# Kernel optimization log

Hardware: AMD Instinct MI355X
Metric: run time of the kernel (lower is better)

## Reference

```python
import jax, jax.numpy as jnp
import numpy as np

N = 50000      # nodes
E = 800000     # edges (avg degree 16)
IN = 256       # in_dim == heads*hidden (so DGL residual is Identity)
H = 4          # heads
D = 64         # hidden_dim / out_dim per head
EPS = 1e-5
NEG_SLOPE_ATTN = 0.2   # DGL GATConv edge-attention leaky_relu slope
NEG_SLOPE_ACT = 0.01   # F.leaky_relu default


def gat_conv(x, src, dst, W, al, ar, b, act):
    # x: [N, H*D], W: [H*D, H*D], al/ar: [H, D], b: [H*D]
    feat = (x @ W).reshape(N, H, D)                       # [N,H,D]
    el = jnp.sum(feat * al, axis=-1)                      # [N,H]
    er = jnp.sum(feat * ar, axis=-1)                      # [N,H]
    e = jax.nn.leaky_relu(el[src] + er[dst], NEG_SLOPE_ATTN)  # [E,H]
    # segment softmax over incoming edges per destination node
    m = jax.ops.segment_max(e, dst, num_segments=N)       # [N,H]
    m = jnp.where(jnp.isfinite(m), m, 0.0)                # nodes with no in-edges
    ee = jnp.exp(e - m[dst])                              # [E,H]
    denom = jax.ops.segment_sum(ee, dst, num_segments=N)  # [N,H]
    alpha = ee / jnp.maximum(denom[dst], 1e-9)            # [E,H]
    msg = feat[src] * alpha[:, :, None]                   # [E,H,D]
    rst = jax.ops.segment_sum(msg, dst, num_segments=N)   # [N,H,D]
    rst = rst + x.reshape(N, H, D)                        # identity residual (dims match)
    rst = rst + b.reshape(1, H, D)
    if act:
        rst = jax.nn.leaky_relu(rst, NEG_SLOPE_ACT)
    return rst


def batch_norm(h, gamma, beta):
    # BatchNorm1d in training mode: batch statistics over node dim
    mu = jnp.mean(h, axis=0)
    var = jnp.var(h, axis=0)
    return (h - mu) * jax.lax.rsqrt(var + EPS) * gamma + beta


def setup_inputs():
    key = jax.random.key(0)
    ks = jax.random.split(key, 18)
    s = 1.0 / np.sqrt(IN)
    inp = {
        'x': jax.random.normal(ks[0], (N, IN), jnp.float32),
        'src': jax.random.randint(ks[1], (E,), 0, N),
        'dst': jax.random.randint(ks[2], (E,), 0, N),
    }
    names = ['W1', 'al1', 'ar1', 'b1', 'W2', 'al2', 'ar2', 'b2', 'W3', 'al3', 'ar3', 'b3']
    shapes = [(IN, H * D), (H, D), (H, D), (H * D,)] * 3
    for i, (nm, sh) in enumerate(zip(names, shapes)):
        inp[nm] = jax.random.normal(ks[3 + i], sh, jnp.float32) * s
    inp['g1'] = jnp.ones((H * D,), jnp.float32)
    inp['be1'] = jnp.zeros((H * D,), jnp.float32)
    inp['g2'] = jnp.ones((H * D,), jnp.float32)
    inp['be2'] = jnp.zeros((H * D,), jnp.float32)
    return inp


def reference(x, src, dst, W1, al1, ar1, b1, W2, al2, ar2, b2, W3, al3, ar3, b3, g1, be1, g2, be2):
    h = gat_conv(x, src, dst, W1, al1, ar1, b1, act=True).reshape(N, H * D)
    h = batch_norm(h, g1, be1)
    h = gat_conv(h, src, dst, W2, al2, ar2, b2, act=True).reshape(N, H * D)
    h = batch_norm(h, g2, be2)
    h = gat_conv(h, src, dst, W3, al3, ar3, b3, act=False)   # [N,H,D]
    return h.mean(axis=1)                                    # [N,D]
```

## Files before the change

kernel.cpp:

```cpp
#include <hip/hip_runtime.h>

constexpr int NN = 50000;
constexpr int NE = 800000;
constexpr float SLOPE_A = 0.2f;
constexpr float SLOPE_R = 0.01f;
constexpr int SCB = 196;

typedef __attribute__((ext_vector_type(8))) short bf16x8;
typedef __attribute__((ext_vector_type(4))) float f32x4;

__device__ __forceinline__ unsigned short f2bf(float f) {
    union { float f; unsigned u; } v; v.f = f;
    unsigned u = v.u;
    unsigned r = u + 0x7fffu + ((u >> 16) & 1u);
    return (unsigned short)(r >> 16);
}
__device__ __forceinline__ float bf2f(unsigned short s) {
    union { unsigned u; float f; } v; v.u = ((unsigned)s) << 16;
    return v.f;
}
__device__ __forceinline__ float bflo(unsigned u) {
    union { unsigned u; float f; } v; v.u = u << 16; return v.f;
}
__device__ __forceinline__ float bfhi(unsigned u) {
    union { unsigned u; float f; } v; v.u = u & 0xffff0000u; return v.f;
}

__global__ void k_hist(const int* __restrict__ dst, int* __restrict__ cnt) {
    int i = blockIdx.x * 256 + threadIdx.x;
    if (i < NE) atomicAdd(&cnt[dst[i]], 1);
}

__global__ void k_scan1(const int* __restrict__ cnt, int* __restrict__ loc,
                        int* __restrict__ bsum) {
    __shared__ int sh[256];
    int t = threadIdx.x;
    int i = blockIdx.x * 256 + t;
    int v = (i < NN) ? cnt[i] : 0;
    sh[t] = v;
    __syncthreads();
    for (int off = 1; off < 256; off <<= 1) {
        int tmp = (t >= off) ? sh[t - off] : 0;
        __syncthreads();
        sh[t] += tmp;
        __syncthreads();
    }
    loc[i] = sh[t] - v;
    if (t == 255) bsum[blockIdx.x] = sh[255];
}

__global__ void k_scan2(const int* __restrict__ bsum, int* __restrict__ boff,
                        int* __restrict__ rowptr) {
    __shared__ int sh[256];
    int t = threadIdx.x;
    int v = (t < SCB) ? bsum[t] : 0;
    sh[t] = v;
    __syncthreads();
    for (int off = 1; off < 256; off <<= 1) {
        int tmp = (t >= off) ? sh[t - off] : 0;
        __syncthreads();
        sh[t] += tmp;
        __syncthreads();
    }
    if (t < SCB) boff[t] = sh[t] - v;
    if (t == 255) rowptr[NN] = sh[255];
}

__global__ void k_scan3(const int* __restrict__ loc, const int* __restrict__ boff,
                        int* __restrict__ rowptr, int* __restrict__ cursor) {
    int i = blockIdx.x * 256 + threadIdx.x;
    if (i < NN) {
        int r = loc[i] + boff[blockIdx.x];
        rowptr[i] = r;
        cursor[i] = r;
    }
}

__global__ void k_scatter(const int* __restrict__ src, const int* __restrict__ dst,
                          int* __restrict__ cursor, int* __restrict__ ssrc) {
    int i = blockIdx.x * 256 + threadIdx.x;
    if (i < NE) {
        int d = dst[i];
        int pos = atomicAdd(&cursor[d], 1);
        ssrc[pos] = src[i];
    }
}

__global__ void k_fold(const float* __restrict__ W, const float* __restrict__ sc,
                       const float* __restrict__ sh, const float* __restrict__ al,
                       const float* __restrict__ ar, unsigned short* __restrict__ Wfrag,
                       float* __restrict__ cvec, unsigned short* __restrict__ wlrfrag,
                       float* __restrict__ offlr, int has_bn) {
    int b = blockIdx.x;
    if (b < 32) {
        int gid = b * 256 + threadIdx.x;
        int lane = gid & 63;
        int frag = gid >> 6;
        int j = frag & 3, kc = (frag >> 2) & 7, w = frag >> 5;
        int mm = lane & 15, q = lane >> 4;
        int n = 64 * w + 16 * j + mm;
        int k0 = kc * 32 + q * 8;
        unsigned short o[8];
#pragma unroll
        for (int t = 0; t < 8; t++) {
            float wv = W[(size_t)(k0 + t) * 256 + n];
            if (sc) wv *= sc[k0 + t];
            o[t] = f2bf(wv);
        }
        *(uint4*)(Wfrag + (size_t)gid * 8) = *(const uint4*)o;
    } else if (has_bn && b < 288) {
        __shared__ float red[256];
        int n = b - 32, k = threadIdx.x;
        red[k] = sh[k] * W[(size_t)k * 256 + n];
        __syncthreads();
        for (int off = 128; off > 0; off >>= 1) {
            if (k < off) red[k] += red[k + off];
            __syncthreads();
        }
        if (k == 0) cvec[n] = red[0];
    } else {
        int n = b - (has_bn ? 288 : 32);
        int h = n >> 1;
        const float* a = (n & 1) ? ar : al;
        int k = threadIdx.x;
        float raw = 0.f;
#pragma unroll 8
        for (int d = 0; d < 64; d++)
            raw += W[(size_t)k * 256 + 64 * h + d] * a[h * 64 + d];
        float val = (sc ? sc[k] : 1.f) * raw;
        int kc = k >> 5, rem = k & 31, q = rem >> 3, t = rem & 7;
        wlrfrag[kc * 512 + (q * 16 + n) * 8 + t] = f2bf(val);
        wlrfrag[kc * 512 + (q * 16 + n + 8) * 8 + t] = 0;
        __shared__ float red[256];
        red[k] = sh ? sh[k] * raw : 0.f;
        __syncthreads();
        for (int off = 128; off > 0; off >>= 1) {
            if (k < off) red[k] += red[k + off];
            __syncthreads();
        }
        if (k == 0) offlr[n] = red[0];
    }
}

__launch_bounds__(256)
__global__ void k_gemm(const void* __restrict__ Araw, int af32,
                       const unsigned short* __restrict__ Wfrag,
                       const float* __restrict__ cvec,
                       const unsigned short* __restrict__ wlrfrag,
                       const float* __restrict__ offlr,
                       unsigned short* __restrict__ feat16, float* __restrict__ el,
                       float* __restrict__ er) {
    constexpr int AP = 264;
    __shared__ __align__(16) unsigned short Alds[64 * AP];
    const int tid = threadIdx.x;
    const int rowbase = blockIdx.x * 64;

    if (af32) {
        const float* A = (const float*)Araw;
        int r = tid >> 6;
        int c4 = tid & 63;
        for (int it = 0; it < 16; it++) {
            int rr = it * 4 + r;
            int gr = rowbase + rr;
            float4 v = make_float4(0.f, 0.f, 0.f, 0.f);
            if (gr < NN) v = *(const float4*)(A + (size_t)gr * 256 + c4 * 4);
            ushort4 pv;
            pv.x = f2bf(v.x); pv.y = f2bf(v.y); pv.z = f2bf(v.z); pv.w = f2bf(v.w);
            *(ushort4*)(&Alds[rr * AP + c4 * 4]) = pv;
        }
    } else {
        const unsigned short* A = (const unsigned short*)Araw;
        for (int it = 0; it < 8; it++) {
            int idx = it * 256 + tid;
            int rr = idx >> 5;
            int c16 = idx & 31;
            int gr = rowbase + rr;
            uint4 v = make_uint4(0u, 0u, 0u, 0u);
            if (gr < NN) v = *(const uint4*)(A + (size_t)gr * 256 + c16 * 8);
            *(uint4*)(&Alds[rr * AP + c16 * 8]) = v;
        }
    }
    __syncthreads();

    f32x4 acc[4][4];
    for (int i = 0; i < 4; i++)
        for (int j = 0; j < 4; j++)
            acc[i][j] = (f32x4){0.f, 0.f, 0.f, 0.f};
    f32x4 accLR[4];
    for (int i = 0; i < 4; i++) accLR[i] = (f32x4){0.f, 0.f, 0.f, 0.f};

    const int lane = tid & 63, w = tid >> 6;
    const int mm = lane & 15, q = lane >> 4;

    const unsigned short* bbase = Wfrag + ((size_t)w * 8 * 4) * 512 + (size_t)lane * 8;

#pragma unroll
    for (int kc = 0; kc < 8; kc++) {
        bf16x8 a[4], b[4];
        for (int i = 0; i < 4; i++)
            a[i] = *(const bf16x8*)(&Alds[(16 * i + mm) * AP + kc * 32 + q * 8]);
        for (int j = 0; j < 4; j++)
            b[j] = *(const bf16x8*)(bbase + (size_t)(kc * 4 + j) * 512);
        for (int i = 0; i < 4; i++)
            for (int j = 0; j < 4; j++)
                acc[i][j] = __builtin_amdgcn_mfma_f32_16x16x32_bf16(a[i], b[j], acc[i][j], 0, 0, 0);
        if (w == 0) {
            bf16x8 blr = *(const bf16x8*)(wlrfrag + kc * 512 + lane * 8);
            for (int i = 0; i < 4; i++)
                accLR[i] = __builtin_amdgcn_mfma_f32_16x16x32_bf16(a[i], blr, accLR[i], 0, 0, 0);
        }
    }
    __syncthreads();

    if (cvec) {
        float cv[4];
        for (int j = 0; j < 4; j++) cv[j] = cvec[64 * w + 16 * j + mm];
        for (int i = 0; i < 4; i++)
            for (int j = 0; j < 4; j++)
                for (int r = 0; r < 4; r++)
                    acc[i][j][r] += cv[j];
    }

    if (w == 0 && mm < 8) {
        float off = offlr[mm];
        int h = mm >> 1;
        float* dstp = (mm & 1) ? er : el;
        for (int i = 0; i < 4; i++)
            for (int r = 0; r < 4; r++) {
                int gr = rowbase + 16 * i + q * 4 + r;
                if (gr < NN) dstp[gr * 4 + h] = accLR[i][r] + off;
            }
    }

    for (int i = 0; i < 4; i++)
        for (int j = 0; j < 4; j++) {
            int gc = 64 * w + 16 * j + mm;
            for (int r = 0; r < 4; r++) {
                int rr = 16 * i + q * 4 + r;
                Alds[rr * AP + gc] = f2bf(acc[i][j][r]);
            }
        }
    __syncthreads();
    for (int it = 0; it < 8; it++) {
        int idx = it * 256 + tid;
        int rr = idx >> 5;
        int c16 = idx & 31;
        int gr = rowbase + rr;
        if (gr < NN)
            *(uint4*)(feat16 + (size_t)gr * 256 + c16 * 8) = *(const uint4*)(&Alds[rr * AP + c16 * 8]);
    }
}

__launch_bounds__(256)
__global__ void k_agg(const unsigned short* __restrict__ feat16,
                      const float* __restrict__ el, const float* __restrict__ er,
                      const int* __restrict__ rowptr, const int* __restrict__ ssrc,
                      const unsigned short* __restrict__ residh, const float* __restrict__ residf,
                      const float* __restrict__ bnscale, const float* __restrict__ bnshift,
                      int use_bn, const float* __restrict__ bias, int act,
                      unsigned short* __restrict__ outh, float* __restrict__ outf,
                      int final_mean) {
    int n = __builtin_amdgcn_readfirstlane(blockIdx.x * 4 + (threadIdx.x >> 6));
    int l = threadIdx.x & 63;
    int p = l >> 5;
    int q = l & 31;
    int c8 = q * 8;
    int hh = q >> 3;
    int wh = l & 3;
    int we = l >> 2;
    int beg = rowptr[n], end = rowptr[n + 1];
    float er_w = er[n * 4 + wh];

    float d = 0.f;
    float acc[8];
#pragma unroll
    for (int k = 0; k < 8; k++) acc[k] = 0.f;

    for (int e = beg; e < end; e += 16) {
        int widx = e + we;
        bool wv = widx < end;
        int sw = ssrc[wv ? widx : beg];
        float a = el[sw * 4 + wh];
        float sc = a + er_w;
        sc = (sc > 0.f) ? sc : SLOPE_A * sc;
        float wl = wv ? __expf(sc) : 0.f;

        int ss[8];
#pragma unroll
        for (int t = 0; t < 8; t++) {
            int idx = e + 2 * t + p;
            ss[t] = ssrc[(idx < end) ? idx : beg];
        }
        uint4 ff[8];
#pragma unroll
        for (int t = 0; t < 8; t++)
            ff[t] = *(const uint4*)(feat16 + (size_t)ss[t] * 256 + c8);

#pragma unroll
        for (int t = 0; t < 8; t++) {
            float w = __shfl(wl, (2 * t + p) * 4 + hh, 64);
            d += w;
            acc[0] += bflo(ff[t].x) * w; acc[1] += bfhi(ff[t].x) * w;
            acc[2] += bflo(ff[t].y) * w; acc[3] += bfhi(ff[t].y) * w;
            acc[4] += bflo(ff[t].z) * w; acc[5] += bfhi(ff[t].z) * w;
            acc[6] += bflo(ff[t].w) * w; acc[7] += bfhi(ff[t].w) * w;
        }
    }

    d += __shfl_xor(d, 32, 64);
#pragma unroll
    for (int k = 0; k < 8; k++) acc[k] += __shfl_xor(acc[k], 32, 64);

    float invd = 1.f / fmaxf(d, 1e-9f);
#pragma unroll
    for (int k = 0; k < 8; k++) acc[k] *= invd;

    float r[8];
    if (residf) {
        float4 r0 = *(const float4*)(residf + (size_t)n * 256 + c8);
        float4 r1 = *(const float4*)(residf + (size_t)n * 256 + c8 + 4);
        r[0] = r0.x; r[1] = r0.y; r[2] = r0.z; r[3] = r0.w;
        r[4] = r1.x; r[5] = r1.y; r[6] = r1.z; r[7] = r1.w;
    } else {
        uint4 rv = *(const uint4*)(residh + (size_t)n * 256 + c8);
        r[0] = bflo(rv.x); r[1] = bfhi(rv.x);
        r[2] = bflo(rv.y); r[3] = bfhi(rv.y);
        r[4] = bflo(rv.z); r[5] = bfhi(rv.z);
        r[6] = bflo(rv.w); r[7] = bfhi(rv.w);
    }

    if (use_bn) {
        float4 s0 = *(const float4*)(bnscale + c8);
        float4 s1 = *(const float4*)(bnscale + c8 + 4);
        float4 h0 = *(const float4*)(bnshift + c8);
        float4 h1 = *(const float4*)(bnshift + c8 + 4);
        r[0] = r[0] * s0.x + h0.x; r[1] = r[1] * s0.y + h0.y;
        r[2] = r[2] * s0.z + h0.z; r[3] = r[3] * s0.w + h0.w;
        r[4] = r[4] * s1.x + h1.x; r[5] = r[5] * s1.y + h1.y;
        r[6] = r[6] * s1.z + h1.z; r[7] = r[7] * s1.w + h1.w;
    }
    {
        float4 b0 = *(const float4*)(bias + c8);
        float4 b1 = *(const float4*)(bias + c8 + 4);
        acc[0] += r[0] + b0.x; acc[1] += r[1] + b0.y;
        acc[2] += r[2] + b0.z; acc[3] += r[3] + b0.w;
        acc[4] += r[4] + b1.x; acc[5] += r[5] + b1.y;
        acc[6] += r[6] + b1.z; acc[7] += r[7] + b1.w;
    }
    if (act) {
#pragma unroll
        for (int k = 0; k < 8; k++) acc[k] = (acc[k] > 0.f) ? acc[k] : SLOPE_R * acc[k];
    }

    if (!final_mean) {
        if (p == 0) {
            uint4 o;
            o.x = (unsigned)f2bf(acc[0]) | ((unsigned)f2bf(acc[1]) << 16);
            o.y = (unsigned)f2bf(acc[2]) | ((unsigned)f2bf(acc[3]) << 16);
            o.z = (unsigned)f2bf(acc[4]) | ((unsigned)f2bf(acc[5]) << 16);
            o.w = (unsigned)f2bf(acc[6]) | ((unsigned)f2bf(acc[7]) << 16);
            *(uint4*)(outh + (size_t)n * 256 + c8) = o;
        }
    } else {
#pragma unroll
        for (int k = 0; k < 8; k++) {
            acc[k] += __shfl_xor(acc[k], 8, 64);
            acc[k] += __shfl_xor(acc[k], 16, 64);
        }
        if (p == 0 && q < 8) {
            float4 o0 = make_float4(acc[0] * 0.25f, acc[1] * 0.25f, acc[2] * 0.25f, acc[3] * 0.25f);
            float4 o1 = make_float4(acc[4] * 0.25f, acc[5] * 0.25f, acc[6] * 0.25f, acc[7] * 0.25f);
            *(float4*)(outf + (size_t)n * 64 + c8) = o0;
            *(float4*)(outf + (size_t)n * 64 + c8 + 4) = o1;
        }
    }
}

__global__ void k_bnstats(const unsigned short* __restrict__ hh, float* __restrict__ pbuf) {
    __shared__ float ps[8 * 256];
    __shared__ float ps2[8 * 256];
    int t = threadIdx.x, b = blockIdx.x;
    int r8 = t >> 5, c32 = t & 31;
    int r0 = b * 196, r1 = min(r0 + 196, NN);
    float s[8], s2[8];
#pragma unroll
    for (int e = 0; e < 8; e++) { s[e] = 0.f; s2[e] = 0.f; }
    for (int r = r0 + r8; r < r1; r += 8) {
        uint4 v = *(const uint4*)(hh + (size_t)r * 256 + c32 * 8);
        const unsigned short* pv = (const unsigned short*)&v;
#pragma unroll
        for (int e = 0; e < 8; e++) {
            float f = bf2f(pv[e]);
            s[e] += f; s2[e] += f * f;
        }
    }
#pragma unroll
    for (int e = 0; e < 8; e++) {
        ps[r8 * 256 + c32 * 8 + e] = s[e];
        ps2[r8 * 256 + c32 * 8 + e] = s2[e];
    }
    __syncthreads();
    float ts = 0.f, ts2 = 0.f;
    for (int g = 0; g < 8; g++) { ts += ps[g * 256 + t]; ts2 += ps2[g * 256 + t]; }
    pbuf[b * 512 + t] = ts;
    pbuf[b * 512 + 256 + t] = ts2;
}

__global__ void k_bnfinal(const float* __restrict__ pbuf, const float* __restrict__ g,
                          const float* __restrict__ be, float* __restrict__ scale,
                          float* __restrict__ shift) {
    int t = threadIdx.x;
    float s = 0.f, s2 = 0.f;
    for (int b = 0; b < 256; b++) {
        s += pbuf[b * 512 + t];
        s2 += pbuf[b * 512 + 256 + t];
    }
    float mu = s * (1.f / NN);
    float var = s2 * (1.f / NN) - mu * mu;
    float rs = rsqrtf(var + 1e-5f);
    float sc = rs * g[t];
    scale[t] = sc;
    shift[t] = be[t] - mu * sc;
}

extern "C" void kernel_launch(void* const* d_in, const int* in_sizes, int n_in,
                              void* d_out, int out_size, void* d_ws, size_t ws_size,
                              hipStream_t stream) {
    const float* x   = (const float*)d_in[0];
    const int* src   = (const int*)d_in[1];
    const int* dst   = (const int*)d_in[2];
    const float* W1  = (const float*)d_in[3];
    const float* al1 = (const float*)d_in[4];
    const float* ar1 = (const float*)d_in[5];
    const float* b1  = (const float*)d_in[6];
    const float* W2  = (const float*)d_in[7];
    const float* al2 = (const float*)d_in[8];
    const float* ar2 = (const float*)d_in[9];
    const float* b2  = (const float*)d_in[10];
    const float* W3  = (const float*)d_in[11];
    const float* al3 = (const float*)d_in[12];
    const float* ar3 = (const float*)d_in[13];
    const float* b3  = (const float*)d_in[14];
    const float* g1  = (const float*)d_in[15];
    const float* be1 = (const float*)d_in[16];
    const float* g2  = (const float*)d_in[17];
    const float* be2 = (const float*)d_in[18];
    float* out = (float*)d_out;

    char* ws = (char*)d_ws;
    size_t off = 0;
    auto alloc = [&](size_t bytes) {
        void* p = ws + off;
        off += (bytes + 255) & ~(size_t)255;
        return p;
    };
    int* rowptr = (int*)alloc((NN + 1) * sizeof(int));
    int* cursor = (int*)alloc(NN * sizeof(int));
    int* cnt    = (int*)alloc(SCB * 256 * sizeof(int));
    int* loc    = (int*)alloc(SCB * 256 * sizeof(int));
    int* bsum   = (int*)alloc(SCB * sizeof(int));
    int* boff   = (int*)alloc(SCB * sizeof(int));
    int* ssrc   = (int*)alloc(NE * sizeof(int));
    unsigned short* feat16 = (unsigned short*)alloc((size_t)NN * 256 * sizeof(unsigned short));
    unsigned short* hbuf   = (unsigned short*)alloc((size_t)NN * 256 * sizeof(unsigned short));
    float* el   = (float*)alloc((size_t)NN * 4 * sizeof(float));
    float* er   = (float*)alloc((size_t)NN * 4 * sizeof(float));
    unsigned short* Wfrag1  = (unsigned short*)alloc(65536 * sizeof(unsigned short));
    unsigned short* Wfrag2  = (unsigned short*)alloc(65536 * sizeof(unsigned short));
    unsigned short* wlrfrag = (unsigned short*)alloc(4096 * sizeof(unsigned short));
    float* offlr   = (float*)alloc(16 * sizeof(float));
    float* cvec    = (float*)alloc(256 * sizeof(float));
    float* pbuf    = (float*)alloc(256 * 512 * sizeof(float));
    float* bnscale = (float*)alloc(256 * sizeof(float));
    float* bnshift = (float*)alloc(256 * sizeof(float));

    hipMemsetAsync(cnt, 0, NN * sizeof(int), stream);
    k_hist<<<(NE + 255) / 256, 256, 0, stream>>>(dst, cnt);
    k_scan1<<<SCB, 256, 0, stream>>>(cnt, loc, bsum);
    k_scan2<<<1, 256, 0, stream>>>(bsum, boff, rowptr);
    k_scan3<<<SCB, 256, 0, stream>>>(loc, boff, rowptr, cursor);
    k_scatter<<<(NE + 255) / 256, 256, 0, stream>>>(src, dst, cursor, ssrc);
    k_fold<<<40, 256, 0, stream>>>(W1, nullptr, nullptr, al1, ar1,
                                   Wfrag1, nullptr, wlrfrag, offlr, 0);

    const int GB = (NN + 63) / 64;
    const int NB = NN / 4;

    k_gemm<<<GB, 256, 0, stream>>>(x, 1, Wfrag1, nullptr, wlrfrag, offlr, feat16, el, er);
    k_agg<<<NB, 256, 0, stream>>>(feat16, el, er, rowptr, ssrc, nullptr, x,
                                  nullptr, nullptr, 0, b1, 1, hbuf, nullptr, 0);
    k_bnstats<<<256, 256, 0, stream>>>(hbuf, pbuf);
    k_bnfinal<<<1, 256, 0, stream>>>(pbuf, g1, be1, bnscale, bnshift);
    k_fold<<<296, 256, 0, stream>>>(W2, bnscale, bnshift, al2, ar2,
                                    Wfrag2, cvec, wlrfrag, offlr, 1);

    k_gemm<<<GB, 256, 0, stream>>>(hbuf, 0, Wfrag2, cvec, wlrfrag, offlr, feat16, el, er);
    k_agg<<<NB, 256, 0, stream>>>(feat16, el, er, rowptr, ssrc, hbuf, nullptr,
                                  bnscale, bnshift, 1, b2, 1, hbuf, nullptr, 0);
    k_bnstats<<<256, 256, 0, stream>>>(hbuf, pbuf);
    k_bnfinal<<<1, 256, 0, stream>>>(pbuf, g2, be2, bnscale, bnshift);
    k_fold<<<296, 256, 0, stream>>>(W3, bnscale, bnshift, al3, ar3,
                                    Wfrag2, cvec, wlrfrag, offlr, 1);

    k_gemm<<<GB, 256, 0, stream>>>(hbuf, 0, Wfrag2, cvec, wlrfrag, offlr, feat16, el, er);
    k_agg<<<NB, 256, 0, stream>>>(feat16, el, er, rowptr, ssrc, hbuf, nullptr,
                                  bnscale, bnshift, 1, b3, 0, nullptr, out, 1);
}
```

Before: 571.6 us.

## Split GAT aggregation into per-head column slices with compact indices

The aggregation kernel is restructured so each block handles 16 nodes for one 32-column slice, with the 8 slices of a node group on consecutive block indices. Each lane group computes its own head's attention weights, so the cross-lane shuffle of weights goes away. The el/er logits are stored head-major, and the sorted source indices are stored as 16-bit values since N fits. The goal is more parallelism, better L2 locality on feature gathers, and less index traffic. In exchange, index and logit reads are repeated across the slices, and the final head-mean becomes float atomics into a zero-initialised output.

```diff
diff --git a/kernel.cpp b/kernel.cpp
--- a/kernel.cpp
+++ b/kernel.cpp
@@ -77,12 +77,12 @@
 }
 
 __global__ void k_scatter(const int* __restrict__ src, const int* __restrict__ dst,
-                          int* __restrict__ cursor, int* __restrict__ ssrc) {
+                          int* __restrict__ cursor, unsigned short* __restrict__ ssrc) {
     int i = blockIdx.x * 256 + threadIdx.x;
     if (i < NE) {
         int d = dst[i];
         int pos = atomicAdd(&cursor[d], 1);
-        ssrc[pos] = src[i];
+        ssrc[pos] = (unsigned short)src[i];
     }
 }
 
@@ -228,7 +228,7 @@
         for (int i = 0; i < 4; i++)
             for (int r = 0; r < 4; r++) {
                 int gr = rowbase + 16 * i + q * 4 + r;
-                if (gr < NN) dstp[gr * 4 + h] = accLR[i][r] + off;
+                if (gr < NN) dstp[h * NN + gr] = accLR[i][r] + off;
             }
     }
 
@@ -252,126 +252,125 @@
 }
 
 __launch_bounds__(256)
-__global__ void k_agg(const unsigned short* __restrict__ feat16,
-                      const float* __restrict__ el, const float* __restrict__ er,
-                      const int* __restrict__ rowptr, const int* __restrict__ ssrc,
-                      const unsigned short* __restrict__ residh, const float* __restrict__ residf,
-                      const float* __restrict__ bnscale, const float* __restrict__ bnshift,
-                      int use_bn, const float* __restrict__ bias, int act,
-                      unsigned short* __restrict__ outh, float* __restrict__ outf,
-                      int final_mean) {
-    int n = __builtin_amdgcn_readfirstlane(blockIdx.x * 4 + (threadIdx.x >> 6));
+__global__ void k_aggs(const unsigned short* __restrict__ feat16,
+                       const float* __restrict__ el, const float* __restrict__ er,
+                       const int* __restrict__ rowptr, const unsigned short* __restrict__ ssrc,
+                       const unsigned short* __restrict__ residh, const float* __restrict__ residf,
+                       const float* __restrict__ bnscale, const float* __restrict__ bnshift,
+                       int use_bn, const float* __restrict__ bias, int act,
+                       unsigned short* __restrict__ outh, float* __restrict__ outf,
+                       int final_mean) {
+    int b = blockIdx.x;
+    int slice = b & 7;
+    int ng = b >> 3;
     int l = threadIdx.x & 63;
-    int p = l >> 5;
-    int q = l & 31;
-    int c8 = q * 8;
-    int hh = q >> 3;
-    int wh = l & 3;
-    int we = l >> 2;
+    int w = threadIdx.x >> 6;
+    int j = l >> 4;
+    int r = l & 15;
+    int es = r >> 2;
+    int ck = r & 3;
+    int n = ng * 16 + w * 4 + j;
+    int h = slice >> 1;
+    int coff = slice * 32 + ck * 8;
+
     int beg = rowptr[n], end = rowptr[n + 1];
-    float er_w = er[n * 4 + wh];
+    float er_h = er[h * NN + n];
+    const float* elh = el + h * NN;
 
     float d = 0.f;
     float acc[8];
 #pragma unroll
     for (int k = 0; k < 8; k++) acc[k] = 0.f;
 
-    for (int e = beg; e < end; e += 16) {
-        int widx = e + we;
-        bool wv = widx < end;
-        int sw = ssrc[wv ? widx : beg];
-        float a = el[sw * 4 + wh];
-        float sc = a + er_w;
-        sc = (sc > 0.f) ? sc : SLOPE_A * sc;
-        float wl = wv ? __expf(sc) : 0.f;
-
-        int ss[8];
-#pragma unroll
-        for (int t = 0; t < 8; t++) {
-            int idx = e + 2 * t + p;
+    for (int e0 = beg; e0 < end; e0 += 16) {
+        int ss[4];
+#pragma unroll
+        for (int t = 0; t < 4; t++) {
+            int idx = e0 + t * 4 + es;
             ss[t] = ssrc[(idx < end) ? idx : beg];
         }
-        uint4 ff[8];
-#pragma unroll
-        for (int t = 0; t < 8; t++)
-            ff[t] = *(const uint4*)(feat16 + (size_t)ss[t] * 256 + c8);
-
-#pragma unroll
-        for (int t = 0; t < 8; t++) {
-            float w = __shfl(wl, (2 * t + p) * 4 + hh, 64);
-            d += w;
-            acc[0] += bflo(ff[t].x) * w; acc[1] += bfhi(ff[t].x) * w;
-            acc[2] += bflo(ff[t].y) * w; acc[3] += bfhi(ff[t].y) * w;
-            acc[4] += bflo(ff[t].z) * w; acc[5] += bfhi(ff[t].z) * w;
-            acc[6] += bflo(ff[t].w) * w; acc[7] += bfhi(ff[t].w) * w;
-        }
-    }
-
-    d += __shfl_xor(d, 32, 64);
-#pragma unroll
-    for (int k = 0; k < 8; k++) acc[k] += __shfl_xor(acc[k], 32, 64);
+        float aa[4];
+#pragma unroll
+        for (int t = 0; t < 4; t++) aa[t] = elh[ss[t]];
+        uint4 ff[4];
+#pragma unroll
+        for (int t = 0; t < 4; t++)
+            ff[t] = *(const uint4*)(feat16 + (size_t)ss[t] * 256 + coff);
+#pragma unroll
+        for (int t = 0; t < 4; t++) {
+            int idx = e0 + t * 4 + es;
+            float sc = aa[t] + er_h;
+            sc = (sc > 0.f) ? sc : SLOPE_A * sc;
+            float wg = (idx < end) ? __expf(sc) : 0.f;
+            d += wg;
+            acc[0] += bflo(ff[t].x) * wg; acc[1] += bfhi(ff[t].x) * wg;
+            acc[2] += bflo(ff[t].y) * wg; acc[3] += bfhi(ff[t].y) * wg;
+            acc[4] += bflo(ff[t].z) * wg; acc[5] += bfhi(ff[t].z) * wg;
+            acc[6] += bflo(ff[t].w) * wg; acc[7] += bfhi(ff[t].w) * wg;
+        }
+    }
+
+    d += __shfl_xor(d, 4, 64);
+    d += __shfl_xor(d, 8, 64);
+#pragma unroll
+    for (int k = 0; k < 8; k++) {
+        acc[k] += __shfl_xor(acc[k], 4, 64);
+        acc[k] += __shfl_xor(acc[k], 8, 64);
+    }
 
     float invd = 1.f / fmaxf(d, 1e-9f);
 #pragma unroll
     for (int k = 0; k < 8; k++) acc[k] *= invd;
 
-    float r[8];
+    float rr[8];
     if (residf) {
-        float4 r0 = *(const float4*)(residf + (size_t)n * 256 + c8);
-        float4 r1 = *(const float4*)(residf + (size_t)n * 256 + c8 + 4);
-        r[0] = r0.x; r[1] = r0.y; r[2] = r0.z; r[3] = r0.w;
-        r[4] = r1.x; r[5] = r1.y; r[6] = r1.z; r[7] = r1.w;
+        float4 r0 = *(const float4*)(residf + (size_t)n * 256 + coff);
+        float4 r1 = *(const float4*)(residf + (size_t)n * 256 + coff + 4);
+        rr[0] = r0.x; rr[1] = r0.y; rr[2] = r0.z; rr[3] = r0.w;
+        rr[4] = r1.x; rr[5] = r1.y; rr[6] = r1.z; rr[7] = r1.w;
     } else {
-        uint4 rv = *(const uint4*)(residh + (size_t)n * 256 + c8);
-        r[0] = bflo(rv.x); r[1] = bfhi(rv.x);
-        r[2] = bflo(rv.y); r[3] = bfhi(rv.y);
-        r[4] = bflo(rv.z); r[5] = bfhi(rv.z);
-        r[6] = bflo(rv.w); r[7] = bfhi(rv.w);
-    }
-
+        uint4 rv = *(const uint4*)(residh + (size_t)n * 256 + coff);
+        rr[0] = bflo(rv.x); rr[1] = bfhi(rv.x);
+        rr[2] = bflo(rv.y); rr[3] = bfhi(rv.y);
+        rr[4] = bflo(rv.z); rr[5] = bfhi(rv.z);
+        rr[6] = bflo(rv.w); rr[7] = bfhi(rv.w);
+    }
     if (use_bn) {
-        float4 s0 = *(const float4*)(bnscale + c8);
-        float4 s1 = *(const float4*)(bnscale + c8 + 4);
-        float4 h0 = *(const float4*)(bnshift + c8);
-        float4 h1 = *(const float4*)(bnshift + c8 + 4);
-        r[0] = r[0] * s0.x + h0.x; r[1] = r[1] * s0.y + h0.y;
-        r[2] = r[2] * s0.z + h0.z; r[3] = r[3] * s0.w + h0.w;
-        r[4] = r[4] * s1.x + h1.x; r[5] = r[5] * s1.y + h1.y;
-        r[6] = r[6] * s1.z + h1.z; r[7] = r[7] * s1.w + h1.w;
+        float4 s0 = *(const float4*)(bnscale + coff);
+        float4 s1 = *(const float4*)(bnscale + coff + 4);
+        float4 h0 = *(const float4*)(bnshift + coff);
+        float4 h1 = *(const float4*)(bnshift + coff + 4);
+        rr[0] = rr[0] * s0.x + h0.x; rr[1] = rr[1] * s0.y + h0.y;
+        rr[2] = rr[2] * s0.z + h0.z; rr[3] = rr[3] * s0.w + h0.w;
+        rr[4] = rr[4] * s1.x + h1.x; rr[5] = rr[5] * s1.y + h1.y;
+        rr[6] = rr[6] * s1.z + h1.z; rr[7] = rr[7] * s1.w + h1.w;
     }
     {
-        float4 b0 = *(const float4*)(bias + c8);
-        float4 b1 = *(const float4*)(bias + c8 + 4);
-        acc[0] += r[0] + b0.x; acc[1] += r[1] + b0.y;
-        acc[2] += r[2] + b0.z; acc[3] += r[3] + b0.w;
-        acc[4] += r[4] + b1.x; acc[5] += r[5] + b1.y;
-        acc[6] += r[6] + b1.z; acc[7] += r[7] + b1.w;
+        float4 b0 = *(const float4*)(bias + coff);
+        float4 b1 = *(const float4*)(bias + coff + 4);
+        acc[0] += rr[0] + b0.x; acc[1] += rr[1] + b0.y;
+        acc[2] += rr[2] + b0.z; acc[3] += rr[3] + b0.w;
+        acc[4] += rr[4] + b1.x; acc[5] += rr[5] + b1.y;
+        acc[6] += rr[6] + b1.z; acc[7] += rr[7] + b1.w;
     }
     if (act) {
 #pragma unroll
         for (int k = 0; k < 8; k++) acc[k] = (acc[k] > 0.f) ? acc[k] : SLOPE_R * acc[k];
     }
 
-    if (!final_mean) {
-        if (p == 0) {
+    if (es == 0) {
+        if (!final_mean) {
             uint4 o;
             o.x = (unsigned)f2bf(acc[0]) | ((unsigned)f2bf(acc[1]) << 16);
             o.y = (unsigned)f2bf(acc[2]) | ((unsigned)f2bf(acc[3]) << 16);
             o.z = (unsigned)f2bf(acc[4]) | ((unsigned)f2bf(acc[5]) << 16);
             o.w = (unsigned)f2bf(acc[6]) | ((unsigned)f2bf(acc[7]) << 16);
-            *(uint4*)(outh + (size_t)n * 256 + c8) = o;
-        }
-    } else {
-#pragma unroll
-        for (int k = 0; k < 8; k++) {
-            acc[k] += __shfl_xor(acc[k], 8, 64);
-            acc[k] += __shfl_xor(acc[k], 16, 64);
-        }
-        if (p == 0 && q < 8) {
-            float4 o0 = make_float4(acc[0] * 0.25f, acc[1] * 0.25f, acc[2] * 0.25f, acc[3] * 0.25f);
-            float4 o1 = make_float4(acc[4] * 0.25f, acc[5] * 0.25f, acc[6] * 0.25f, acc[7] * 0.25f);
-            *(float4*)(outf + (size_t)n * 64 + c8) = o0;
-            *(float4*)(outf + (size_t)n * 64 + c8 + 4) = o1;
+            *(uint4*)(outh + (size_t)n * 256 + coff) = o;
+        } else {
+            int dd = (slice & 1) * 32 + ck * 8;
+#pragma unroll
+            for (int k = 0; k < 8; k++)
+                atomicAdd(outf + (size_t)n * 64 + dd + k, 0.25f * acc[k]);
         }
     }
 }
@@ -460,7 +459,7 @@
     int* loc    = (int*)alloc(SCB * 256 * sizeof(int));
     int* bsum   = (int*)alloc(SCB * sizeof(int));
     int* boff   = (int*)alloc(SCB * sizeof(int));
-    int* ssrc   = (int*)alloc(NE * sizeof(int));
+    unsigned short* ssrc = (unsigned short*)alloc(NE * sizeof(unsigned short));
     unsigned short* feat16 = (unsigned short*)alloc((size_t)NN * 256 * sizeof(unsigned short));
     unsigned short* hbuf   = (unsigned short*)alloc((size_t)NN * 256 * sizeof(unsigned short));
     float* el   = (float*)alloc((size_t)NN * 4 * sizeof(float));
@@ -482,27 +481,28 @@
     k_scatter<<<(NE + 255) / 256, 256, 0, stream>>>(src, dst, cursor, ssrc);
     k_fold<<<40, 256, 0, stream>>>(W1, nullptr, nullptr, al1, ar1,
                                    Wfrag1, nullptr, wlrfrag, offlr, 0);
+    hipMemsetAsync(out, 0, (size_t)NN * 64 * sizeof(float), stream);
 
     const int GB = (NN + 63) / 64;
-    const int NB = NN / 4;
+    const int AB = 8 * (NN / 16);
 
     k_gemm<<<GB, 256, 0, stream>>>(x, 1, Wfrag1, nullptr, wlrfrag, offlr, feat16, el, er);
-    k_agg<<<NB, 256, 0, stream>>>(feat16, el, er, rowptr, ssrc, nullptr, x,
-                                  nullptr, nullptr, 0, b1, 1, hbuf, nullptr, 0);
+    k_aggs<<<AB, 256, 0, stream>>>(feat16, el, er, rowptr, ssrc, nullptr, x,
+                                   nullptr, nullptr, 0, b1, 1, hbuf, nullptr, 0);
     k_bnstats<<<256, 256, 0, stream>>>(hbuf, pbuf);
     k_bnfinal<<<1, 256, 0, stream>>>(pbuf, g1, be1, bnscale, bnshift);
     k_fold<<<296, 256, 0, stream>>>(W2, bnscale, bnshift, al2, ar2,
                                     Wfrag2, cvec, wlrfrag, offlr, 1);
 
     k_gemm<<<GB, 256, 0, stream>>>(hbuf, 0, Wfrag2, cvec, wlrfrag, offlr, feat16, el, er);
-    k_agg<<<NB, 256, 0, stream>>>(feat16, el, er, rowptr, ssrc, hbuf, nullptr,
-                                  bnscale, bnshift, 1, b2, 1, hbuf, nullptr, 0);
+    k_aggs<<<AB, 256, 0, stream>>>(feat16, el, er, rowptr, ssrc, hbuf, nullptr,
+                                   bnscale, bnshift, 1, b2, 1, hbuf, nullptr, 0);
     k_bnstats<<<256, 256, 0, stream>>>(hbuf, pbuf);
     k_bnfinal<<<1, 256, 0, stream>>>(pbuf, g2, be2, bnscale, bnshift);
     k_fold<<<296, 256, 0, stream>>>(W3, bnscale, bnshift, al3, ar3,
                                     Wfrag2, cvec, wlrfrag, offlr, 1);
 
     k_gemm<<<GB, 256, 0, stream>>>(hbuf, 0, Wfrag2, cvec, wlrfrag, offlr, feat16, el, er);
-    k_agg<<<NB, 256, 0, stream>>>(feat16, el, er, rowptr, ssrc, hbuf, nullptr,
-                                  bnscale, bnshift, 1, b3, 0, nullptr, out, 1);
-}
+    k_aggs<<<AB, 256, 0, stream>>>(feat16, el, er, rowptr, ssrc, hbuf, nullptr,
+                                   bnscale, bnshift, 1, b3, 0, nullptr, out, 1);
+}
```

New measurement: 881.7 us. 1.54x slower.

## Compress edge source indices to 16-bit and compute attention weights per lane

Applied to the files above, without the earlier changes.

Sorted source indices are now stored as unsigned short, which is valid because the node count is below 65536; this halves the index traffic in the scatter and aggregation kernels. The aggregation loop now processes 8 edges per iteration instead of 16. Each lane loads el for its own edge and head and computes the exp weight itself, replacing the separate weight pass and the cross-lane shuffles. The residual load is moved ahead of the loop. In exchange there are redundant el loads and exps across lanes, and fewer feature gathers in flight per iteration, which may reduce latency hiding.

```diff
diff --git a/kernel.cpp b/kernel.cpp
--- a/kernel.cpp
+++ b/kernel.cpp
@@ -77,12 +77,12 @@
 }
 
 __global__ void k_scatter(const int* __restrict__ src, const int* __restrict__ dst,
-                          int* __restrict__ cursor, int* __restrict__ ssrc) {
+                          int* __restrict__ cursor, unsigned short* __restrict__ ssrc) {
     int i = blockIdx.x * 256 + threadIdx.x;
     if (i < NE) {
         int d = dst[i];
         int pos = atomicAdd(&cursor[d], 1);
-        ssrc[pos] = src[i];
+        ssrc[pos] = (unsigned short)src[i];
     }
 }
 
@@ -254,7 +254,7 @@
 __launch_bounds__(256)
 __global__ void k_agg(const unsigned short* __restrict__ feat16,
                       const float* __restrict__ el, const float* __restrict__ er,
-                      const int* __restrict__ rowptr, const int* __restrict__ ssrc,
+                      const int* __restrict__ rowptr, const unsigned short* __restrict__ ssrc,
                       const unsigned short* __restrict__ residh, const float* __restrict__ residf,
                       const float* __restrict__ bnscale, const float* __restrict__ bnshift,
                       int use_bn, const float* __restrict__ bias, int act,
@@ -266,54 +266,8 @@
     int q = l & 31;
     int c8 = q * 8;
     int hh = q >> 3;
-    int wh = l & 3;
-    int we = l >> 2;
     int beg = rowptr[n], end = rowptr[n + 1];
-    float er_w = er[n * 4 + wh];
-
-    float d = 0.f;
-    float acc[8];
-#pragma unroll
-    for (int k = 0; k < 8; k++) acc[k] = 0.f;
-
-    for (int e = beg; e < end; e += 16) {
-        int widx = e + we;
-        bool wv = widx < end;
-        int sw = ssrc[wv ? widx : beg];
-        float a = el[sw * 4 + wh];
-        float sc = a + er_w;
-        sc = (sc > 0.f) ? sc : SLOPE_A * sc;
-        float wl = wv ? __expf(sc) : 0.f;
-
-        int ss[8];
-#pragma unroll
-        for (int t = 0; t < 8; t++) {
-            int idx = e + 2 * t + p;
-            ss[t] = ssrc[(idx < end) ? idx : beg];
-        }
-        uint4 ff[8];
-#pragma unroll
-        for (int t = 0; t < 8; t++)
-            ff[t] = *(const uint4*)(feat16 + (size_t)ss[t] * 256 + c8);
-
-#pragma unroll
-        for (int t = 0; t < 8; t++) {
-            float w = __shfl(wl, (2 * t + p) * 4 + hh, 64);
-            d += w;
-            acc[0] += bflo(ff[t].x) * w; acc[1] += bfhi(ff[t].x) * w;
-            acc[2] += bflo(ff[t].y) * w; acc[3] += bfhi(ff[t].y) * w;
-            acc[4] += bflo(ff[t].z) * w; acc[5] += bfhi(ff[t].z) * w;
-            acc[6] += bflo(ff[t].w) * w; acc[7] += bfhi(ff[t].w) * w;
-        }
-    }
-
-    d += __shfl_xor(d, 32, 64);
-#pragma unroll
-    for (int k = 0; k < 8; k++) acc[k] += __shfl_xor(acc[k], 32, 64);
-
-    float invd = 1.f / fmaxf(d, 1e-9f);
-#pragma unroll
-    for (int k = 0; k < 8; k++) acc[k] *= invd;
+    float erh = er[n * 4 + hh];
 
     float r[8];
     if (residf) {
@@ -328,6 +282,47 @@
         r[4] = bflo(rv.z); r[5] = bfhi(rv.z);
         r[6] = bflo(rv.w); r[7] = bfhi(rv.w);
     }
+
+    float d = 0.f;
+    float acc[8];
+#pragma unroll
+    for (int k = 0; k < 8; k++) acc[k] = 0.f;
+
+    for (int e = beg; e < end; e += 8) {
+        int ss[4];
+#pragma unroll
+        for (int j = 0; j < 4; j++) {
+            int idx = e + 2 * j + p;
+            ss[j] = ssrc[(idx < end) ? idx : beg];
+        }
+        float aa[4];
+#pragma unroll
+        for (int j = 0; j < 4; j++)
+            aa[j] = el[ss[j] * 4 + hh];
+        uint4 ff[4];
+#pragma unroll
+        for (int j = 0; j < 4; j++)
+            ff[j] = *(const uint4*)(feat16 + (size_t)ss[j] * 256 + c8);
+#pragma unroll
+        for (int j = 0; j < 4; j++) {
+            float sc = aa[j] + erh;
+            sc = (sc > 0.f) ? sc : SLOPE_A * sc;
+            float w = ((e + 2 * j + p) < end) ? __expf(sc) : 0.f;
+            d += w;
+            acc[0] += bflo(ff[j].x) * w; acc[1] += bfhi(ff[j].x) * w;
+            acc[2] += bflo(ff[j].y) * w; acc[3] += bfhi(ff[j].y) * w;
+            acc[4] += bflo(ff[j].z) * w; acc[5] += bfhi(ff[j].z) * w;
+            acc[6] += bflo(ff[j].w) * w; acc[7] += bfhi(ff[j].w) * w;
+        }
+    }
+
+    d += __shfl_xor(d, 32, 64);
+#pragma unroll
+    for (int k = 0; k < 8; k++) acc[k] += __shfl_xor(acc[k], 32, 64);
+
+    float invd = 1.f / fmaxf(d, 1e-9f);
+#pragma unroll
+    for (int k = 0; k < 8; k++) acc[k] *= invd;
 
     if (use_bn) {
         float4 s0 = *(const float4*)(bnscale + c8);
@@ -460,7 +455,7 @@
     int* loc    = (int*)alloc(SCB * 256 * sizeof(int));
     int* bsum   = (int*)alloc(SCB * sizeof(int));
     int* boff   = (int*)alloc(SCB * sizeof(int));
-    int* ssrc   = (int*)alloc(NE * sizeof(int));
+    unsigned short* ssrc = (unsigned short*)alloc(NE * sizeof(unsigned short));
     unsigned short* feat16 = (unsigned short*)alloc((size_t)NN * 256 * sizeof(unsigned short));
     unsigned short* hbuf   = (unsigned short*)alloc((size_t)NN * 256 * sizeof(unsigned short));
     float* el   = (float*)alloc((size_t)NN * 4 * sizeof(float));
```

After: 547.1 us, median of 2. -4.3%, faster.
